# Kernel tuning notes

Hardware: AMD Instinct MI355X
Metric: run time of the kernel (lower is better)

The kernel has to match this reference:

```python
import jax, jax.numpy as jnp
import numpy as np

NUM_HEADS = 16
WINDOW = 16  # hard-coded in module; half-window = 8


def sliding_mask(seq_len):
    # mask[i, j] = 0 if j in [i - W//2, i + W//2], else -inf  (additive)
    i = jnp.arange(seq_len)[:, None]
    j = jnp.arange(seq_len)[None, :]
    return jnp.where(jnp.abs(i - j) <= WINDOW // 2, 0.0, -jnp.inf).astype(jnp.float32)


def setup_inputs() -> dict:
    key = jax.random.key(0)
    k1, k2, k3 = jax.random.split(key, 3)
    B, S, D = 2, 2048, 1024
    scale = 1.0 / np.sqrt(D)
    return {
        "input_embeddings": jax.random.normal(k1, (B, S, D), dtype=jnp.float32),
        "token_ids": jax.random.randint(k2, (B, S), 0, 32000, dtype=jnp.int64),
        # nn.MultiheadAttention params: packed in_proj [3D, D] + bias, out_proj [D, D] + bias
        "w_qkv": jax.random.normal(jax.random.fold_in(k3, 0), (3 * D, D), dtype=jnp.float32) * scale,
        "b_qkv": jnp.zeros((3 * D,), dtype=jnp.float32),
        "w_out": jax.random.normal(jax.random.fold_in(k3, 1), (D, D), dtype=jnp.float32) * scale,
        "b_out": jnp.zeros((D,), dtype=jnp.float32),
    }


def reference(input_embeddings, token_ids, w_qkv, b_qkv, w_out, b_out):
    B, S, D = input_embeddings.shape
    H = NUM_HEADS
    hd = D // H
    # packed QKV projection (torch in_proj): [B, S, 3D]
    qkv = input_embeddings @ w_qkv.T + b_qkv
    q, k, v = jnp.split(qkv, 3, axis=-1)
    # [B, H, S, hd]
    q = q.reshape(B, S, H, hd).transpose(0, 2, 1, 3)
    k = k.reshape(B, S, H, hd).transpose(0, 2, 1, 3)
    v = v.reshape(B, S, H, hd).transpose(0, 2, 1, 3)
    scores = jnp.einsum("bhqd,bhkd->bhqk", q, k) / jnp.sqrt(jnp.asarray(hd, q.dtype))
    scores = scores + sliding_mask(S)  # broadcast additive [S, S] mask
    attn = jax.nn.softmax(scores, axis=-1)
    ctx = jnp.einsum("bhqk,bhkd->bhqd", attn, v)
    ctx = ctx.transpose(0, 2, 1, 3).reshape(B, S, D)
    return ctx @ w_out.T + b_out
```

## Files before the change

kernel.cpp:

```cpp
#include <hip/hip_runtime.h>
#include <stdint.h>


typedef __bf16 bf16_t;
typedef bf16_t bf16x8 __attribute__((ext_vector_type(8)));
typedef unsigned short u16x8 __attribute__((ext_vector_type(8)));
typedef float f32x4 __attribute__((ext_vector_type(4)));

#define GLD16(g, l)                                                        \
  __builtin_amdgcn_global_load_lds(                                        \
      (const __attribute__((address_space(1))) void*)(g),                  \
      (__attribute__((address_space(3))) void*)(l), 16, 0, 0)

__device__ __forceinline__ unsigned short f2bf(float f) {
  unsigned int u = __float_as_uint(f);
  u += 0x7FFFu + ((u >> 16) & 1u);
  return (unsigned short)(u >> 16);
}

__device__ __forceinline__ bf16x8 ld16(const unsigned short* p) {
  return __builtin_bit_cast(bf16x8, *reinterpret_cast<const u16x8*>(p));
}

__global__ void cvt_all(const float* __restrict__ x, const float* __restrict__ wq,
                        const float* __restrict__ wo, unsigned short* __restrict__ xb,
                        unsigned short* __restrict__ wqb,
                        unsigned short* __restrict__ wob) {
  const int N0 = 1048576, N1 = 786432, N2 = 262144;
  for (int i = blockIdx.x * blockDim.x + threadIdx.x; i < N0 + N1 + N2;
       i += gridDim.x * blockDim.x) {
    const float4* src;
    unsigned short* dst;
    int j;
    if (i < N0) { src = (const float4*)x; dst = xb; j = i; }
    else if (i < N0 + N1) { src = (const float4*)wq; dst = wqb; j = i - N0; }
    else { src = (const float4*)wo; dst = wob; j = i - N0 - N1; }
    const float4 f = src[j];
    ushort4 o;
    o.x = f2bf(f.x); o.y = f2bf(f.y); o.z = f2bf(f.z); o.w = f2bf(f.w);
    reinterpret_cast<ushort4*>(dst)[j] = o;
  }
}

__global__ __launch_bounds__(256) void gemm_qkv(
    const unsigned short* __restrict__ A,
    const unsigned short* __restrict__ Bt,
    const float* __restrict__ bias,
    unsigned short* __restrict__ Cq, unsigned short* __restrict__ Ck,
    unsigned short* __restrict__ Cv) {
  __shared__ unsigned short sA[3][4096];
  __shared__ unsigned short sB[3][4096];

  const int K = 1024;
  const int tid = threadIdx.x;
  const int wave = tid >> 6;
  const int lane = tid & 63;
  const int m0 = blockIdx.x << 7;
  const int n0 = blockIdx.y << 7;

  const int wr = wave >> 1;
  const int wc = wave & 1;

  f32x4 acc[4][4] = {};

  const int srow = (wave << 4) + (lane >> 2);
  const int sslot = (((lane & 3) ^ ((lane >> 3) & 3)) << 3);
  const unsigned short* Ag = A + (size_t)(m0 + srow) * K + sslot;
  const unsigned short* Bg = Bt + (size_t)(n0 + srow) * K + sslot;
  const int wdst = wave * 512;

  auto stage = [&](int t, int b) {
#pragma unroll
    for (int r = 0; r < 2; ++r) {
      GLD16(Ag + (size_t)(r * 64) * K + t * 32, &sA[b][r * 2048 + wdst]);
      GLD16(Bg + (size_t)(r * 64) * K + t * 32, &sB[b][r * 2048 + wdst]);
    }
  };

  stage(0, 0);
  stage(1, 1);
  stage(2, 2);

  const int qr = lane & 15;
  const int kg = lane >> 4;
  const int geff8 = ((kg ^ ((qr >> 1) & 3)) << 3);
  const int ar = wr * 64 + qr;
  const int br = wc * 64 + qr;

  for (int t = 0; t < 32; ++t) {
    if (t < 30)
      asm volatile("s_waitcnt vmcnt(8)" ::: "memory");
    else if (t == 30)
      asm volatile("s_waitcnt vmcnt(4)" ::: "memory");
    else
      asm volatile("s_waitcnt vmcnt(0)" ::: "memory");
    __builtin_amdgcn_s_barrier();

    const int b = t % 3;
    const unsigned short* sAb = sA[b];
    const unsigned short* sBb = sB[b];

    bf16x8 af[4], bf[4];
#pragma unroll
    for (int f = 0; f < 4; ++f) {
      af[f] = ld16(&sAb[(ar + f * 16) * 32 + geff8]);
      bf[f] = ld16(&sBb[(br + f * 16) * 32 + geff8]);
    }
    asm volatile("s_waitcnt lgkmcnt(0)" ::: "memory");
    __builtin_amdgcn_sched_barrier(0);
    __builtin_amdgcn_s_barrier();

    if (t + 3 < 32) stage(t + 3, b);

    __builtin_amdgcn_s_setprio(1);
#pragma unroll
    for (int i = 0; i < 4; ++i)
#pragma unroll
      for (int j = 0; j < 4; ++j)
        acc[i][j] = __builtin_amdgcn_mfma_f32_16x16x32_bf16(af[i], bf[j],
                                                            acc[i][j], 0, 0, 0);
    __builtin_amdgcn_s_setprio(0);
  }

#pragma unroll
  for (int i = 0; i < 4; ++i) {
    const int row0 = m0 + wr * 64 + i * 16 + ((lane >> 4) << 2);
#pragma unroll
    for (int j = 0; j < 4; ++j) {
      const int col = n0 + wc * 64 + j * 16 + (lane & 15);
      const float bb = bias[col];
#pragma unroll
      for (int r = 0; r < 4; ++r) {
        const int mm = row0 + r;
        const float val = acc[i][j][r] + bb;
        const int b2 = mm >> 11, s = mm & 2047;
        const int which = col >> 10, nn = col & 1023;
        const int h = nn >> 6, d = nn & 63;
        const int bh = (b2 << 4) + h;
        const unsigned short vb = f2bf(val);
        if (which == 0)
          Cq[((size_t)(bh * 2048 + s)) * 64 + d] = vb;
        else if (which == 1)
          Ck[((size_t)(bh * 2048 + s)) * 64 + d] = vb;
        else
          Cv[((size_t)(bh * 64 + d)) * 2048 + s] = vb;
      }
    }
  }
}

__global__ __launch_bounds__(256, 2) void gemm_bt(
    const unsigned short* __restrict__ A,
    const unsigned short* __restrict__ Bt,
    const float* __restrict__ bias,
    float* __restrict__ Cp, int M, int N, int K, int gny) {
  __shared__ unsigned short sA[2][8192];
  __shared__ unsigned short sB[2][8192];

  const int tid = threadIdx.x;
  const int wave = tid >> 6;
  const int lane = tid & 63;

  const int nwg = gridDim.x;
  const int bid = blockIdx.x;
  const int cw = (nwg >> 3) / gny;
  const int xcd = bid & 7;
  const int idx = bid >> 3;
  const int m0 = (xcd * cw + idx % cw) * 128;
  const int n0 = (idx / cw) * 128;

  const int wr = wave >> 1;
  const int wc = wave & 1;

  f32x4 acc[4][4] = {};

  const int srow = (wave << 3) + (lane >> 3);
  const int sslot = ((lane & 7) ^ (lane >> 3)) << 3;
  const unsigned short* Ag = A + (size_t)(m0 + srow) * K + sslot;
  const unsigned short* Bg = Bt + (size_t)(n0 + srow) * K + sslot;
  const int wdst = wave * 512;

  const int T = K >> 6;

  auto stage = [&](int t, int b) {
#pragma unroll
    for (int r = 0; r < 4; ++r) {
      GLD16(Ag + (size_t)(r * 32) * K + t * 64, &sA[b][r * 2048 + wdst]);
      GLD16(Bg + (size_t)(r * 32) * K + t * 64, &sB[b][r * 2048 + wdst]);
    }
  };

  stage(0, 0);
  stage(1, 1);

  const int kg = lane >> 4;
  const int l7 = lane & 7;
  const int arr = wr * 64 + (lane & 15);
  const int brr = wc * 64 + (lane & 15);

  for (int t = 0; t < T; ++t) {
    if (t < T - 1)
      asm volatile("s_waitcnt vmcnt(8)" ::: "memory");
    else
      asm volatile("s_waitcnt vmcnt(0)" ::: "memory");
    __builtin_amdgcn_s_barrier();

    const int b = t & 1;
    const unsigned short* sAb = sA[b];
    const unsigned short* sBb = sB[b];
    bf16x8 af[2][4], bfr[2][4];
#pragma unroll
    for (int st = 0; st < 2; ++st) {
#pragma unroll
      for (int f = 0; f < 4; ++f) {
        const int se = ((st << 2) | kg) ^ l7;
        af[st][f] = ld16(&sAb[(arr + f * 16) * 64 + (se << 3)]);
        bfr[st][f] = ld16(&sBb[(brr + f * 16) * 64 + (se << 3)]);
      }
    }
    asm volatile("s_waitcnt lgkmcnt(0)" ::: "memory");
    __builtin_amdgcn_sched_barrier(0);
    __builtin_amdgcn_s_barrier();

    if (t + 2 < T) stage(t + 2, b);

#pragma unroll
    for (int st = 0; st < 2; ++st)
#pragma unroll
      for (int i = 0; i < 4; ++i)
#pragma unroll
        for (int j = 0; j < 4; ++j)
          acc[i][j] = __builtin_amdgcn_mfma_f32_16x16x32_bf16(
              af[st][i], bfr[st][j], acc[i][j], 0, 0, 0);
  }

#pragma unroll
  for (int i = 0; i < 4; ++i) {
    const int row0 = m0 + wr * 64 + i * 16 + ((lane >> 4) << 2);
#pragma unroll
    for (int j = 0; j < 4; ++j) {
      const int col = n0 + wc * 64 + j * 16 + (lane & 15);
      const float bb = bias[col];
#pragma unroll
      for (int r = 0; r < 4; ++r)
        Cp[(size_t)(row0 + r) * N + col] = acc[i][j][r] + bb;
    }
  }
}

__global__ __launch_bounds__(256) void attn_mfma(
    const unsigned short* __restrict__ Qb, const unsigned short* __restrict__ Kb,
    const unsigned short* __restrict__ Vt, unsigned short* __restrict__ ctx) {
  __shared__ unsigned short P[4][16][40];
  const int wave = threadIdx.x >> 6;
  const int lane = threadIdx.x & 63;
  const int gw = (blockIdx.x << 2) + wave;
  const int bh = gw >> 7;
  const int i0 = (gw & 127) << 4;
  const int qr = lane & 15;
  const int kg = lane >> 4;
  const int kc = kg << 3;

  const size_t qbase = ((size_t)(bh * 2048 + i0 + qr)) * 64;
  const bf16x8 aq0 = ld16(Qb + qbase + kc);
  const bf16x8 aq1 = ld16(Qb + qbase + 32 + kc);

  f32x4 sc0 = {0.f, 0.f, 0.f, 0.f}, sc1 = {0.f, 0.f, 0.f, 0.f};
  {
    const int ka0 = i0 - 8 + qr;
    const int ka1 = ka0 + 16;
    const int kcl0 = min(max(ka0, 0), 2047);
    const int kcl1 = min(max(ka1, 0), 2047);
    const unsigned short* K0 = Kb + ((size_t)(bh * 2048 + kcl0)) * 64;
    const unsigned short* K1 = Kb + ((size_t)(bh * 2048 + kcl1)) * 64;
    sc0 = __builtin_amdgcn_mfma_f32_16x16x32_bf16(aq0, ld16(K0 + kc), sc0, 0, 0, 0);
    sc0 = __builtin_amdgcn_mfma_f32_16x16x32_bf16(aq1, ld16(K0 + 32 + kc), sc0, 0, 0, 0);
    sc1 = __builtin_amdgcn_mfma_f32_16x16x32_bf16(aq0, ld16(K1 + kc), sc1, 0, 0, 0);
    sc1 = __builtin_amdgcn_mfma_f32_16x16x32_bf16(aq1, ld16(K1 + 32 + kc), sc1, 0, 0, 0);
  }

  unsigned short* Pw = &P[wave][0][0];
  float lsum[4];
#pragma unroll
  for (int r = 0; r < 4; ++r) {
    const int q = (kg << 2) + r;
    const int key0 = qr, key1 = 16 + qr;
    const int ka0 = i0 - 8 + key0, ka1 = i0 - 8 + key1;
    const bool v0 = (q <= key0) && (key0 <= q + 16) && (ka0 >= 0) && (ka0 < 2048);
    const bool v1 = (q <= key1) && (key1 <= q + 16) && (ka1 >= 0) && (ka1 < 2048);
    const float e0 = v0 ? __expf(sc0[r] * 0.125f) : 0.f;
    const float e1 = v1 ? __expf(sc1[r] * 0.125f) : 0.f;
    Pw[q * 40 + key0] = f2bf(e0);
    Pw[q * 40 + key1] = f2bf(e1);
    float s = e0 + e1;
#pragma unroll
    for (int off = 1; off < 16; off <<= 1) s += __shfl_xor(s, off);
    lsum[r] = s;
  }

  const bf16x8 pa = ld16(&Pw[qr * 40 + kc]);

  const int base_s = min(max(i0 - 8 + kc, 0), 2040);
  f32x4 o[4];
  const f32x4 zero = {0.f, 0.f, 0.f, 0.f};
#pragma unroll
  for (int t2 = 0; t2 < 4; ++t2) {
    const unsigned short* Vr =
        Vt + ((size_t)(bh * 64 + t2 * 16 + qr)) * 2048 + base_s;
    o[t2] = __builtin_amdgcn_mfma_f32_16x16x32_bf16(pa, ld16(Vr), zero, 0, 0, 0);
  }

  const int b = bh >> 4, h = bh & 15;
  float rinv[4];
#pragma unroll
  for (int r = 0; r < 4; ++r) rinv[r] = 1.0f / lsum[r];
#pragma unroll
  for (int t2 = 0; t2 < 4; ++t2) {
#pragma unroll
    for (int r = 0; r < 4; ++r) {
      const int q = (kg << 2) + r;
      const int d = t2 * 16 + qr;
      ctx[((size_t)(b * 2048 + i0 + q)) * 1024 + (h << 6) + d] =
          f2bf(o[t2][r] * rinv[r]);
    }
  }
}

extern "C" void kernel_launch(void* const* d_in, const int* in_sizes, int n_in,
                              void* d_out, int out_size, void* d_ws,
                              size_t ws_size, hipStream_t stream) {
  const float* x = (const float*)d_in[0];
  const float* w_qkv = (const float*)d_in[2];
  const float* b_qkv = (const float*)d_in[3];
  const float* w_out = (const float*)d_in[4];
  const float* b_out = (const float*)d_in[5];
  float* out = (float*)d_out;

  char* ws = (char*)d_ws;
  unsigned short* xb    = (unsigned short*)(ws + 0);
  unsigned short* wqkvb = (unsigned short*)(ws + 8388608);
  unsigned short* woutb = (unsigned short*)(ws + 14680064);
  unsigned short* Qb    = (unsigned short*)(ws + 16777216);
  unsigned short* Kb    = (unsigned short*)(ws + 25165824);
  unsigned short* Vt    = (unsigned short*)(ws + 33554432);
  unsigned short* ctxb  = (unsigned short*)(ws + 41943040);

  cvt_all<<<2048, 256, 0, stream>>>(x, w_qkv, w_out, xb, wqkvb, woutb);

  gemm_qkv<<<dim3(32, 24), 256, 0, stream>>>(xb, wqkvb, b_qkv, Qb, Kb, Vt);

  attn_mfma<<<1024, 256, 0, stream>>>(Qb, Kb, Vt, ctxb);

  gemm_bt<<<256, 256, 0, stream>>>(ctxb, woutb, b_out, out, 4096, 1024, 1024, 8);
}
```

Baseline: 79.21 us.

## Widen QKV GEMM tile to 128x192 and vectorize transposed V stores

```diff
diff --git a/kernel.cpp b/kernel.cpp
--- a/kernel.cpp
+++ b/kernel.cpp
@@ -42,26 +42,25 @@
   }
 }
 
-__global__ __launch_bounds__(256) void gemm_qkv(
+__global__ __launch_bounds__(256, 2) void gemm_qkv(
     const unsigned short* __restrict__ A,
     const unsigned short* __restrict__ Bt,
     const float* __restrict__ bias,
     unsigned short* __restrict__ Cq, unsigned short* __restrict__ Ck,
     unsigned short* __restrict__ Cv) {
-  __shared__ unsigned short sA[3][4096];
-  __shared__ unsigned short sB[3][4096];
+  __shared__ unsigned short smem[30720];
 
   const int K = 1024;
   const int tid = threadIdx.x;
   const int wave = tid >> 6;
   const int lane = tid & 63;
   const int m0 = blockIdx.x << 7;
-  const int n0 = blockIdx.y << 7;
+  const int n0 = blockIdx.y * 192;
 
   const int wr = wave >> 1;
   const int wc = wave & 1;
 
-  f32x4 acc[4][4] = {};
+  f32x4 acc[4][6] = {};
 
   const int srow = (wave << 4) + (lane >> 2);
   const int sslot = (((lane & 3) ^ ((lane >> 3) & 3)) << 3);
@@ -71,10 +70,13 @@
 
   auto stage = [&](int t, int b) {
 #pragma unroll
-    for (int r = 0; r < 2; ++r) {
-      GLD16(Ag + (size_t)(r * 64) * K + t * 32, &sA[b][r * 2048 + wdst]);
-      GLD16(Bg + (size_t)(r * 64) * K + t * 32, &sB[b][r * 2048 + wdst]);
-    }
+    for (int r = 0; r < 2; ++r)
+      GLD16(Ag + (size_t)(r * 64) * K + t * 32,
+            &smem[b * 4096 + r * 2048 + wdst]);
+#pragma unroll
+    for (int r = 0; r < 3; ++r)
+      GLD16(Bg + (size_t)(r * 64) * K + t * 32,
+            &smem[12288 + b * 6144 + r * 2048 + wdst]);
   };
 
   stage(0, 0);
@@ -85,27 +87,26 @@
   const int kg = lane >> 4;
   const int geff8 = ((kg ^ ((qr >> 1) & 3)) << 3);
   const int ar = wr * 64 + qr;
-  const int br = wc * 64 + qr;
+  const int br = wc * 96 + qr;
 
   for (int t = 0; t < 32; ++t) {
     if (t < 30)
-      asm volatile("s_waitcnt vmcnt(8)" ::: "memory");
+      asm volatile("s_waitcnt vmcnt(10)" ::: "memory");
     else if (t == 30)
-      asm volatile("s_waitcnt vmcnt(4)" ::: "memory");
+      asm volatile("s_waitcnt vmcnt(5)" ::: "memory");
     else
       asm volatile("s_waitcnt vmcnt(0)" ::: "memory");
     __builtin_amdgcn_s_barrier();
 
     const int b = t % 3;
-    const unsigned short* sAb = sA[b];
-    const unsigned short* sBb = sB[b];
-
-    bf16x8 af[4], bf[4];
-#pragma unroll
-    for (int f = 0; f < 4; ++f) {
-      af[f] = ld16(&sAb[(ar + f * 16) * 32 + geff8]);
-      bf[f] = ld16(&sBb[(br + f * 16) * 32 + geff8]);
-    }
+    const unsigned short* sAb = &smem[b * 4096];
+    const unsigned short* sBb = &smem[12288 + b * 6144];
+
+    bf16x8 af[4], bf[6];
+#pragma unroll
+    for (int f = 0; f < 4; ++f) af[f] = ld16(&sAb[(ar + f * 16) * 32 + geff8]);
+#pragma unroll
+    for (int j = 0; j < 6; ++j) bf[j] = ld16(&sBb[(br + j * 16) * 32 + geff8]);
     asm volatile("s_waitcnt lgkmcnt(0)" ::: "memory");
     __builtin_amdgcn_sched_barrier(0);
     __builtin_amdgcn_s_barrier();
@@ -116,7 +117,7 @@
 #pragma unroll
     for (int i = 0; i < 4; ++i)
 #pragma unroll
-      for (int j = 0; j < 4; ++j)
+      for (int j = 0; j < 6; ++j)
         acc[i][j] = __builtin_amdgcn_mfma_f32_16x16x32_bf16(af[i], bf[j],
                                                             acc[i][j], 0, 0, 0);
     __builtin_amdgcn_s_setprio(0);
@@ -125,25 +126,26 @@
 #pragma unroll
   for (int i = 0; i < 4; ++i) {
     const int row0 = m0 + wr * 64 + i * 16 + ((lane >> 4) << 2);
-#pragma unroll
-    for (int j = 0; j < 4; ++j) {
-      const int col = n0 + wc * 64 + j * 16 + (lane & 15);
+    const int b2 = row0 >> 11, s0 = row0 & 2047;
+#pragma unroll
+    for (int j = 0; j < 6; ++j) {
+      const int col = n0 + wc * 96 + j * 16 + (lane & 15);
       const float bb = bias[col];
-#pragma unroll
-      for (int r = 0; r < 4; ++r) {
-        const int mm = row0 + r;
-        const float val = acc[i][j][r] + bb;
-        const int b2 = mm >> 11, s = mm & 2047;
-        const int which = col >> 10, nn = col & 1023;
-        const int h = nn >> 6, d = nn & 63;
-        const int bh = (b2 << 4) + h;
-        const unsigned short vb = f2bf(val);
-        if (which == 0)
-          Cq[((size_t)(bh * 2048 + s)) * 64 + d] = vb;
-        else if (which == 1)
-          Ck[((size_t)(bh * 2048 + s)) * 64 + d] = vb;
-        else
-          Cv[((size_t)(bh * 64 + d)) * 2048 + s] = vb;
+      const int which = col >> 10, nn = col & 1023;
+      const int h = nn >> 6, d = nn & 63;
+      const int bh = (b2 << 4) + h;
+      if (which == 2) {
+        ushort4 v4;
+        v4.x = f2bf(acc[i][j][0] + bb);
+        v4.y = f2bf(acc[i][j][1] + bb);
+        v4.z = f2bf(acc[i][j][2] + bb);
+        v4.w = f2bf(acc[i][j][3] + bb);
+        *reinterpret_cast<ushort4*>(&Cv[((size_t)(bh * 64 + d)) * 2048 + s0]) = v4;
+      } else {
+        unsigned short* dst = (which == 0) ? Cq : Ck;
+#pragma unroll
+        for (int r = 0; r < 4; ++r)
+          dst[((size_t)(bh * 2048 + s0 + r)) * 64 + d] = f2bf(acc[i][j][r] + bb);
       }
     }
   }
@@ -347,7 +349,7 @@
 
   cvt_all<<<2048, 256, 0, stream>>>(x, w_qkv, w_out, xb, wqkvb, woutb);
 
-  gemm_qkv<<<dim3(32, 24), 256, 0, stream>>>(xb, wqkvb, b_qkv, Qb, Kb, Vt);
+  gemm_qkv<<<dim3(32, 16), 256, 0, stream>>>(xb, wqkvb, b_qkv, Qb, Kb, Vt);
 
   attn_mfma<<<1024, 256, 0, stream>>>(Qb, Kb, Vt, ctxb);
 
```

Result: faster. 73.90 us (-6.7%).
